# Kernel optimization log

Measured on AMD Instinct MI355X. Metric: run time of the kernel, lower is better.

The kernel has to match this reference:

```python
import jax, jax.numpy as jnp
import numpy as np

D_MODEL = 1024
N_HEADS = 16
HEAD_DIM = D_MODEL // N_HEADS
D_FF = 4 * D_MODEL
EPS = 1e-5


def layer_norm(x, gamma, beta):
    mu = jnp.mean(x, axis=-1, keepdims=True)
    var = jnp.var(x, axis=-1, keepdims=True)
    return (x - mu) * jax.lax.rsqrt(var + EPS) * gamma + beta


def setup_inputs() -> dict:
    key = jax.random.key(0)
    ks = jax.random.split(key, 12)
    B, T, S = 4, 2048, 2048
    s_in = 1.0 / np.sqrt(D_MODEL)
    s_ff = 1.0 / np.sqrt(D_FF)
    return {
        "x": jax.random.normal(ks[0], (B, T, D_MODEL), jnp.float32),
        "context": jax.random.normal(ks[1], (B, S, D_MODEL), jnp.float32),
        "Wq": jax.random.normal(ks[2], (D_MODEL, D_MODEL), jnp.float32) * s_in,
        "Wk": jax.random.normal(ks[3], (D_MODEL, D_MODEL), jnp.float32) * s_in,
        "Wv": jax.random.normal(ks[4], (D_MODEL, D_MODEL), jnp.float32) * s_in,
        "Wo": jax.random.normal(ks[5], (D_MODEL, D_MODEL), jnp.float32) * s_in,
        "W1": jax.random.normal(ks[6], (D_FF, D_MODEL), jnp.float32) * s_in,
        "W2": jax.random.normal(ks[7], (D_MODEL, D_FF), jnp.float32) * s_ff,
        "g1": jnp.ones((D_MODEL,), jnp.float32),
        "b1": jnp.zeros((D_MODEL,), jnp.float32),
        "gc": jnp.ones((D_MODEL,), jnp.float32),
        "bc": jnp.zeros((D_MODEL,), jnp.float32),
        "g2": jnp.ones((D_MODEL,), jnp.float32),
        "b2": jnp.zeros((D_MODEL,), jnp.float32),
    }


def reference(x, context, Wq, Wk, Wv, Wo, W1, W2, g1, b1, gc, bc, g2, b2):
    B, T, C = x.shape
    S = context.shape[1]
    residual = x
    xn = layer_norm(x, g1, b1)
    cn = layer_norm(context, gc, bc)
    # torch Linear: y = x @ W.T ; split heads -> [B, H, T, Dh]
    q = (xn @ Wq.T).reshape(B, T, N_HEADS, HEAD_DIM).transpose(0, 2, 1, 3)
    k = (cn @ Wk.T).reshape(B, S, N_HEADS, HEAD_DIM).transpose(0, 2, 1, 3)
    v = (cn @ Wv.T).reshape(B, S, N_HEADS, HEAD_DIM).transpose(0, 2, 1, 3)
    scale = HEAD_DIM ** (-0.5)
    attn = jax.nn.softmax(jnp.einsum('bhtd,bhsd->bhts', q, k) * scale, axis=-1)
    o = jnp.einsum('bhts,bhsd->bhtd', attn, v).transpose(0, 2, 1, 3).reshape(B, T, C)
    x = residual + o @ Wo.T
    residual = x
    h = layer_norm(x, g2, b2)
    h = jax.nn.gelu(h @ W1.T, approximate=False) @ W2.T
    return residual + h
```

## Files before the change

kernel.cpp:

```cpp
#include <hip/hip_runtime.h>
#include <cstdint>
#include <cstddef>

typedef __attribute__((ext_vector_type(8))) short short8;
typedef __attribute__((ext_vector_type(4))) short short4v;
typedef __attribute__((ext_vector_type(4))) float f32x4;
typedef __attribute__((ext_vector_type(2))) unsigned uint2v;

#define DEV static __device__ __forceinline__

DEV short f2bf(float f) {
    unsigned u = __builtin_bit_cast(unsigned, f);
    unsigned r = (u + 0x7fffu + ((u >> 16) & 1u)) >> 16;
    return (short)r;
}

DEV unsigned cvt_pk_bf16(float a, float b) {
    unsigned r;
    asm("v_cvt_pk_bf16_f32 %0, %1, %2" : "=v"(r) : "v"(a), "v"(b));
    return r;
}

DEV float exp2_hw(float x) {
    float r;
    asm("v_exp_f32 %0, %1" : "=v"(r) : "v"(x));
    return r;
}

DEV float rcp_hw(float x) {
    float r;
    asm("v_rcp_f32 %0, %1" : "=v"(r) : "v"(x));
    return r;
}

DEV float gelu_f(float v) {
    float t  = v * (1.0f + 0.044715f * v * v);
    float e  = exp2_hw(fminf(2.3022082f * t, 126.0f));
    return v * e * rcp_hw(e + 1.0f);
}

DEV void gld16(const void* g, void* l) {
    __builtin_amdgcn_global_load_lds((const __attribute__((address_space(1))) void*)g,
                                     (__attribute__((address_space(3))) void*)l, 16, 0, 0);
}

#define MFMA(c, a, b) asm volatile("v_mfma_f32_16x16x32_bf16 %0, %1, %2, %0" : "+v"(c) : "v"(a), "v"(b))
#define BAR() asm volatile("s_barrier" ::: "memory")

__global__ __launch_bounds__(256) void cvt_weights(
    const float* __restrict__ wq, const float* __restrict__ wk,
    const float* __restrict__ wv, const float* __restrict__ wo,
    const float* __restrict__ w1, const float* __restrict__ w2,
    short* __restrict__ dst) {
    long long gid = (long long)blockIdx.x * 256 + threadIdx.x;
    long long i4 = gid * 4;
    const float* src; long long loc;
    if (i4 < (4LL << 20)) {
        int s = (int)(i4 >> 20);
        src = (s == 0) ? wq : (s == 1) ? wk : (s == 2) ? wv : wo;
        loc = i4 & ((1LL << 20) - 1);
    } else {
        long long r = i4 - (4LL << 20);
        int s = (int)(r >> 22);
        src = s ? w2 : w1;
        loc = r & ((1LL << 22) - 1);
    }
    float4 v = *(const float4*)(src + loc);
    short4v o;
    o.x = f2bf(v.x); o.y = f2bf(v.y); o.z = f2bf(v.z); o.w = f2bf(v.w);
    *(short4v*)(dst + i4) = o;
}

__global__ __launch_bounds__(256) void ln_bf16(const float* __restrict__ x,
                                               const float* __restrict__ g,
                                               const float* __restrict__ bt,
                                               short* __restrict__ out) {
    int row = blockIdx.x;
    const float4* xr = (const float4*)(x + (size_t)row * 1024);
    float4 v = xr[threadIdx.x];
    float s  = v.x + v.y + v.z + v.w;
    float s2 = v.x*v.x + v.y*v.y + v.z*v.z + v.w*v.w;
    #pragma unroll
    for (int m = 1; m < 64; m <<= 1) { s += __shfl_xor(s, m); s2 += __shfl_xor(s2, m); }
    __shared__ float red[8];
    int wid = threadIdx.x >> 6;
    if ((threadIdx.x & 63) == 0) { red[wid] = s; red[4 + wid] = s2; }
    __syncthreads();
    s  = red[0] + red[1] + red[2] + red[3];
    s2 = red[4] + red[5] + red[6] + red[7];
    float mu  = s * (1.0f / 1024.0f);
    float var = fmaxf(s2 * (1.0f / 1024.0f) - mu * mu, 0.0f);
    float rs  = rsqrtf(var + 1e-5f);
    float4 gv = ((const float4*)g)[threadIdx.x];
    float4 bv = ((const float4*)bt)[threadIdx.x];
    short4v o;
    o.x = f2bf((v.x - mu) * rs * gv.x + bv.x);
    o.y = f2bf((v.y - mu) * rs * gv.y + bv.y);
    o.z = f2bf((v.z - mu) * rs * gv.z + bv.z);
    o.w = f2bf((v.w - mu) * rs * gv.w + bv.w);
    *(short4v*)(out + (size_t)row * 1024 + (size_t)threadIdx.x * 4) = o;
}

template<int MODE>
DEV void gemm_core(const short* __restrict__ A, const short* __restrict__ B,
                   void* __restrict__ out, const float* __restrict__ resid,
                   int N, int K, int lda, int ldb, float osc, int bm, int bn) {
    __shared__ short lds[2 * 32768];
    const int tid = threadIdx.x;
    const int row0 = bm << 8, col0 = bn << 8;
    const int wid = tid >> 6, lane = tid & 63;
    const int wm = wid >> 2, wn = wid & 3;
    const int lr = lane & 15, lg = lane >> 4;
    const int NK = K >> 6;

    auto stage = [&](int kt, int which) {
        int d = kt & 1;
        const short* src; int rb; int ld;
        if (which < 2) { src = A; rb = row0; ld = lda; } else { src = B; rb = col0; ld = ldb; }
        int rhalf = (which & 1) << 7;
        short* dst = lds + d * 32768 + which * 8192;
        #pragma unroll
        for (int l = 0; l < 2; ++l) {
            int g = l * 512 + tid;
            int r = g >> 3, c = g & 7;
            gld16(src + (size_t)(rb + rhalf + r) * ld + kt * 64 + ((c ^ (r & 7)) << 3),
                  dst + g * 8);
        }
    };

    f32x4 acc[8][4] = {};

    stage(0, 0); stage(0, 1); stage(0, 2); stage(0, 3);
    if (NK > 1) {
        stage(1, 2); stage(1, 3);
        asm volatile("s_waitcnt vmcnt(4)" ::: "memory");
    } else {
        asm volatile("s_waitcnt vmcnt(0)" ::: "memory");
    }
    BAR();

    const int rBbase = (wn & 1) << 6;
    for (int t = 0; t < NK; ++t) {
        const short* bufA = lds + (t & 1) * 32768 + wm * 8192;
        const short* bufB = lds + (t & 1) * 32768 + 16384 + (wn >> 1) * 8192;
        bool st1 = (t + 1) < NK, st2 = (t + 2) < NK;
        short8 bf2[2][4];

        {
            short8 af[4];
            #pragma unroll
            for (int i = 0; i < 4; ++i) {
                int r = i * 16 + lr;
                af[i] = *(const short8*)(bufA + r * 64 + ((lg ^ (r & 7)) << 3));
            }
            #pragma unroll
            for (int j = 0; j < 4; ++j) {
                int rB = rBbase + j * 16 + lr;
                bf2[0][j] = *(const short8*)(bufB + rB * 64 + ((lg ^ (rB & 7)) << 3));
            }
            if (st1) stage(t + 1, 0);
            BAR();
            __builtin_amdgcn_s_setprio(1);
            #pragma unroll
            for (int i = 0; i < 4; ++i)
                #pragma unroll
                for (int j = 0; j < 4; ++j)
                    MFMA(acc[i][j], af[i], bf2[0][j]);
            __builtin_amdgcn_s_setprio(0);
            BAR();
        }
        {
            short8 af[4];
            #pragma unroll
            for (int i = 0; i < 4; ++i) {
                int r = i * 16 + lr;
                af[i] = *(const short8*)(bufA + r * 64 + (((4 + lg) ^ (r & 7)) << 3));
            }
            #pragma unroll
            for (int j = 0; j < 4; ++j) {
                int rB = rBbase + j * 16 + lr;
                bf2[1][j] = *(const short8*)(bufB + rB * 64 + (((4 + lg) ^ (rB & 7)) << 3));
            }
            if (st1) stage(t + 1, 1);
            BAR();
            __builtin_amdgcn_s_setprio(1);
            #pragma unroll
            for (int i = 0; i < 4; ++i)
                #pragma unroll
                for (int j = 0; j < 4; ++j)
                    MFMA(acc[i][j], af[i], bf2[1][j]);
            __builtin_amdgcn_s_setprio(0);
            BAR();
        }
        {
            short8 af[4];
            #pragma unroll
            for (int i = 0; i < 4; ++i) {
                int r = 64 + i * 16 + lr;
                af[i] = *(const short8*)(bufA + r * 64 + ((lg ^ (r & 7)) << 3));
            }
            if (st2) stage(t + 2, 2);
            BAR();
            __builtin_amdgcn_s_setprio(1);
            #pragma unroll
            for (int i = 0; i < 4; ++i)
                #pragma unroll
                for (int j = 0; j < 4; ++j)
                    MFMA(acc[4 + i][j], af[i], bf2[0][j]);
            __builtin_amdgcn_s_setprio(0);
            BAR();
        }
        {
            short8 af[4];
            #pragma unroll
            for (int i = 0; i < 4; ++i) {
                int r = 64 + i * 16 + lr;
                af[i] = *(const short8*)(bufA + r * 64 + (((4 + lg) ^ (r & 7)) << 3));
            }
            if (st2) stage(t + 2, 3);
            BAR();
            __builtin_amdgcn_s_setprio(1);
            #pragma unroll
            for (int i = 0; i < 4; ++i)
                #pragma unroll
                for (int j = 0; j < 4; ++j)
                    MFMA(acc[4 + i][j], af[i], bf2[1][j]);
            __builtin_amdgcn_s_setprio(0);
            if (st2)      asm volatile("s_waitcnt vmcnt(4)" ::: "memory");
            else if (st1) asm volatile("s_waitcnt vmcnt(0)" ::: "memory");
            BAR();
        }
    }
    asm volatile("s_nop 7\n\ts_nop 7");

    int orow0 = row0 + wm * 128, ocol0 = col0 + wn * 64;
    #pragma unroll
    for (int i = 0; i < 8; ++i)
        #pragma unroll
        for (int j = 0; j < 4; ++j)
            #pragma unroll
            for (int r = 0; r < 4; ++r) {
                int gr = orow0 + i * 16 + lg * 4 + r;
                int gc = ocol0 + j * 16 + lr;
                size_t off = (size_t)gr * N + gc;
                float v = acc[i][j][r];
                if constexpr (MODE == 1) {
                    ((float*)out)[off] = resid ? v + resid[off] : v;
                } else if constexpr (MODE == 2) {
                    ((short*)out)[off] = f2bf(gelu_f(v));
                } else {
                    ((short*)out)[off] = f2bf(v * osc);
                }
            }
}

__global__ __launch_bounds__(512, 2) void gemm_qkv(
    const short* __restrict__ XN, const short* __restrict__ CN,
    const short* __restrict__ Wq, const short* __restrict__ Wk, const short* __restrict__ Wv,
    short* __restrict__ QB, short* __restrict__ KB, short* __restrict__ VT, float qscale) {
    int sid = (blockIdx.x & 7) * 48 + (blockIdx.x >> 3);
    int sub = sid >> 7, i = sid & 127;
    const short *A, *B; short* o; float osc; int N, bm, bn;
    if (sub == 0)      { A = XN; B = Wq; o = QB; osc = qscale; N = 1024; bm = i >> 2; bn = i & 3; }
    else if (sub == 1) { A = CN; B = Wk; o = KB; osc = 1.0f;   N = 1024; bm = i >> 2; bn = i & 3; }
    else               { A = Wv; B = CN; o = VT; osc = 1.0f;   N = 8192; bm = i >> 5; bn = i & 31; }
    gemm_core<3>(A, B, o, nullptr, N, 1024, 1024, 1024, osc, bm, bn);
}

template<int MODE>
__global__ __launch_bounds__(512, 2) void gemm_std(const short* __restrict__ A,
                                                   const short* __restrict__ B,
                                                   void* __restrict__ out,
                                                   const float* __restrict__ resid,
                                                   int N, int K, float osc) {
    int cpx = gridDim.x >> 3;
    int sid = (blockIdx.x & 7) * cpx + (blockIdx.x >> 3);
    int nbn = N >> 8;
    int bm = sid / nbn, bn = sid % nbn;
    gemm_core<MODE>(A, B, out, resid, N, K, K, K, osc, bm, bn);
}

__global__ __launch_bounds__(512, 2) void gemm_ff2(const short* __restrict__ F1,
                                                   const short* __restrict__ W2,
                                                   float* __restrict__ dOut,
                                                   float* __restrict__ P2,
                                                   const float* __restrict__ X2) {
    int sid = (blockIdx.x & 7) * 32 + (blockIdx.x >> 3);
    int h = sid >> 7, i = sid & 127;
    int bm = i >> 2, bn = i & 3;
    const short* A = F1 + h * 2048;
    const short* B = W2 + h * 2048;
    float* o = h ? P2 : dOut;
    const float* r = h ? nullptr : X2;
    gemm_core<1>(A, B, o, r, 1024, 2048, 4096, 4096, 1.0f, bm, bn);
}

__global__ __launch_bounds__(256) void add_f32(float* __restrict__ dst,
                                               const float* __restrict__ src, int n4) {
    int i = blockIdx.x * 256 + threadIdx.x;
    int stride = gridDim.x * 256;
    for (; i < n4; i += stride) {
        float4 a = ((const float4*)dst)[i];
        float4 b = ((const float4*)src)[i];
        a.x += b.x; a.y += b.y; a.z += b.z; a.w += b.w;
        ((float4*)dst)[i] = a;
    }
}

__global__ __launch_bounds__(512) void attn(const short* __restrict__ Q,
                                            const short* __restrict__ K,
                                            const short* __restrict__ Vt,
                                            short* __restrict__ O) {
    __shared__ short lK[2][64 * 64];
    __shared__ short lV[2][64 * 64];
    __shared__ short lP[8][32 * 64];
    int tid = threadIdx.x;
    int sid = (blockIdx.x & 7) * 64 + (blockIdx.x >> 3);
    int bh = sid >> 3, qt = sid & 7;
    int b = bh >> 4, h = bh & 15;
    int wid = tid >> 6, lane = tid & 63;
    int lr = lane & 15, lg = lane >> 4;
    int q0 = qt * 256 + wid * 32;

    short8 qf[2][2];
    #pragma unroll
    for (int fm = 0; fm < 2; ++fm)
        #pragma unroll
        for (int kb = 0; kb < 2; ++kb) {
            size_t roff = (size_t)(b * 2048 + q0 + fm * 16 + lr) * 1024 + h * 64 + kb * 32 + lg * 8;
            qf[fm][kb] = *(const short8*)(Q + roff);
        }

    f32x4 oacc[2][4] = {};
    float mrow[2] = { -1e30f, -1e30f };
    float lrs[2]  = { 0.0f, 0.0f };

    const short* Kb = K + (size_t)(b * 2048) * 1024 + h * 64;
    const short* Vb = Vt + (size_t)(h * 64) * 8192 + b * 2048;
    short* Pw = lP[wid];
    int albase = (lane & 48) >> 2;

    int sr = tid >> 3, sc = tid & 7;
    int ssl = sc ^ (sr & 7);
    auto stage = [&](int st, int d) {
        gld16(Kb + (size_t)(st * 64 + sr) * 1024 + ssl * 8, &lK[d][tid * 8]);
        gld16(Vb + (size_t)sr * 8192 + st * 64 + ssl * 8, &lV[d][tid * 8]);
    };

    stage(0, 0);
    asm volatile("s_waitcnt vmcnt(0)" ::: "memory");
    BAR();

    for (int st = 0; st < 32; ++st) {
        int d = st & 1;
        if (st + 1 < 32) stage(st + 1, d ^ 1);

        f32x4 sc2[4][2] = {};
        #pragma unroll
        for (int kb = 0; kb < 2; ++kb) {
            short8 kf[4];
            #pragma unroll
            for (int fn = 0; fn < 4; ++fn) {
                int kr = fn * 16 + lr;
                kf[fn] = *(const short8*)(lK[d] + kr * 64 + (((kb * 4 + lg) ^ (kr & 7)) << 3));
            }
            #pragma unroll
            for (int fn = 0; fn < 4; ++fn)
                #pragma unroll
                for (int fm = 0; fm < 2; ++fm)
                    MFMA(sc2[fn][fm], kf[fn], qf[fm][kb]);
        }
        asm volatile("s_nop 7\n\ts_nop 7");

        #pragma unroll
        for (int fm = 0; fm < 2; ++fm) {
            float pm = sc2[0][fm][0];
            #pragma unroll
            for (int fn = 0; fn < 4; ++fn)
                #pragma unroll
                for (int r = 0; r < 4; ++r)
                    if (fn | r) pm = fmaxf(pm, sc2[fn][fm][r]);
            pm = fmaxf(pm, __shfl_xor(pm, 16));
            pm = fmaxf(pm, __shfl_xor(pm, 32));

            float mo = mrow[fm];
            float mn = mo;
            float al = 1.0f;
            if (!__all(pm <= mo + 8.0f)) {
                mn = fmaxf(mo, pm);
                al = exp2_hw(mo - mn);
                mrow[fm] = mn;
                #pragma unroll
                for (int r = 0; r < 4; ++r) {
                    float alr = __shfl(al, albase + r);
                    #pragma unroll
                    for (int fn = 0; fn < 4; ++fn) oacc[fm][fn][r] *= alr;
                }
            }

            float p[4][4];
            float ps = 0.0f;
            #pragma unroll
            for (int fn = 0; fn < 4; ++fn)
                #pragma unroll
                for (int r = 0; r < 4; ++r) {
                    p[fn][r] = exp2_hw(sc2[fn][fm][r] - mn);
                    ps += p[fn][r];
                }
            ps += __shfl_xor(ps, 16);
            ps += __shfl_xor(ps, 32);
            lrs[fm] = lrs[fm] * al + ps;

            int pr = fm * 16 + lr;
            int swz = (pr & 7) << 3;
            #pragma unroll
            for (int fn = 0; fn < 4; ++fn) {
                uint2v w;
                w.x = cvt_pk_bf16(p[fn][0], p[fn][1]);
                w.y = cvt_pk_bf16(p[fn][2], p[fn][3]);
                *(uint2v*)(Pw + ((pr * 64 + fn * 16 + lg * 4) ^ swz)) = w;
            }
        }

        #pragma unroll
        for (int kb = 0; kb < 2; ++kb) {
            short8 pa[2], vf[4];
            #pragma unroll
            for (int fm = 0; fm < 2; ++fm) {
                int pr = fm * 16 + lr;
                pa[fm] = *(const short8*)(Pw + pr * 64 + (((kb * 4 + lg) ^ (pr & 7)) << 3));
            }
            #pragma unroll
            for (int fn = 0; fn < 4; ++fn) {
                int vr = fn * 16 + lr;
                vf[fn] = *(const short8*)(lV[d] + vr * 64 + (((kb * 4 + lg) ^ (vr & 7)) << 3));
            }
            #pragma unroll
            for (int fm = 0; fm < 2; ++fm)
                #pragma unroll
                for (int fn = 0; fn < 4; ++fn)
                    MFMA(oacc[fm][fn], pa[fm], vf[fn]);
        }

        asm volatile("s_waitcnt vmcnt(0)" ::: "memory");
        BAR();
    }
    asm volatile("s_nop 7\n\ts_nop 7");

    #pragma unroll
    for (int fm = 0; fm < 2; ++fm)
        #pragma unroll
        for (int r = 0; r < 4; ++r) {
            float linv = __shfl(lrs[fm], albase + r);
            float inv = 1.0f / linv;
            #pragma unroll
            for (int fn = 0; fn < 4; ++fn) {
                size_t off = (size_t)(b * 2048 + q0 + fm * 16 + lg * 4 + r) * 1024 + h * 64 + fn * 16 + lr;
                O[off] = f2bf(oacc[fm][fn][r] * inv);
            }
        }
}

extern "C" void kernel_launch(void* const* d_in, const int* in_sizes, int n_in,
                              void* d_out, int out_size, void* d_ws, size_t ws_size,
                              hipStream_t stream) {
    const float* x   = (const float*)d_in[0];
    const float* ctx = (const float*)d_in[1];
    const float* Wq  = (const float*)d_in[2];
    const float* Wk  = (const float*)d_in[3];
    const float* Wv  = (const float*)d_in[4];
    const float* Wo  = (const float*)d_in[5];
    const float* W1  = (const float*)d_in[6];
    const float* W2  = (const float*)d_in[7];
    const float* g1  = (const float*)d_in[8];
    const float* b1  = (const float*)d_in[9];
    const float* gc  = (const float*)d_in[10];
    const float* bc  = (const float*)d_in[11];
    const float* g2  = (const float*)d_in[12];
    const float* b2  = (const float*)d_in[13];

    char* ws = (char*)d_ws;
    const size_t OFF_W  = 0;
    const size_t OFF_XN = 25165824;
    const size_t OFF_CN = OFF_XN + 16777216;
    const size_t OFF_QB = OFF_CN + 16777216;
    const size_t OFF_KB = OFF_QB + 16777216;
    const size_t OFF_VT = OFF_KB + 16777216;
    const size_t OFF_X2 = OFF_VT + 16777216;
    const size_t OFF_F1 = OFF_X2 + 33554432;

    short* Wb = (short*)(ws + OFF_W);
    short* XN = (short*)(ws + OFF_XN);
    short* CN = (short*)(ws + OFF_CN);
    short* QB = (short*)(ws + OFF_QB);
    short* KB = (short*)(ws + OFF_KB);
    short* VT = (short*)(ws + OFF_VT);
    float* X2 = (float*)(ws + OFF_X2);
    short* F1 = (short*)(ws + OFF_F1);
    short* OB = XN;
    short* H  = CN;
    float* P2 = (float*)(ws + OFF_QB);

    const size_t WQo = 0, WKo = 1048576, WVo = 2097152, WOo = 3145728;
    const size_t W1o = 4194304, W2o = 8388608;
    const float QSCALE = 0.125f * 1.4426950408889634f;

    cvt_weights<<<12288, 256, 0, stream>>>(Wq, Wk, Wv, Wo, W1, W2, Wb);
    ln_bf16<<<8192, 256, 0, stream>>>(x, g1, b1, XN);
    ln_bf16<<<8192, 256, 0, stream>>>(ctx, gc, bc, CN);
    gemm_qkv<<<384, 512, 0, stream>>>(XN, CN, Wb + WQo, Wb + WKo, Wb + WVo, QB, KB, VT, QSCALE);
    attn<<<512, 512, 0, stream>>>(QB, KB, VT, OB);
    gemm_std<1><<<128, 512, 0, stream>>>(OB, Wb + WOo, X2, x, 1024, 1024, 1.0f);
    ln_bf16<<<8192, 256, 0, stream>>>(X2, g2, b2, H);
    gemm_std<2><<<512, 512, 0, stream>>>(H, Wb + W1o, F1, nullptr, 4096, 1024, 1.0f);
    gemm_ff2<<<256, 512, 0, stream>>>(F1, Wb + W2o, (float*)d_out, P2, X2);
    add_f32<<<2048, 256, 0, stream>>>((float*)d_out, P2, 2097152);
}
```

Measured before the change: 469.1 us.

## Halve attention query tile per wave and pass P through register shuffles

The attention kernel now gives each wave 16 query rows instead of 32 and launches twice as many blocks. The softmax probabilities are rearranged into the MFMA A-operand layout with cross-lane shuffles, so the per-wave P tile in LDS and its write/read round trip are gone. Launch bounds request higher occupancy. In exchange, each K/V tile staged in LDS feeds half as many query rows, so K/V global traffic and staging barriers per unit of work double.

```diff
diff --git a/kernel.cpp b/kernel.cpp
--- a/kernel.cpp
+++ b/kernel.cpp
@@ -5,7 +5,7 @@
 typedef __attribute__((ext_vector_type(8))) short short8;
 typedef __attribute__((ext_vector_type(4))) short short4v;
 typedef __attribute__((ext_vector_type(4))) float f32x4;
-typedef __attribute__((ext_vector_type(2))) unsigned uint2v;
+typedef __attribute__((ext_vector_type(4))) unsigned uint4v;
 
 #define DEV static __device__ __forceinline__
 
@@ -307,41 +307,38 @@
     }
 }
 
-__global__ __launch_bounds__(512) void attn(const short* __restrict__ Q,
-                                            const short* __restrict__ K,
-                                            const short* __restrict__ Vt,
-                                            short* __restrict__ O) {
+__global__ __launch_bounds__(512, 6) void attn(const short* __restrict__ Q,
+                                               const short* __restrict__ K,
+                                               const short* __restrict__ Vt,
+                                               short* __restrict__ O) {
     __shared__ short lK[2][64 * 64];
     __shared__ short lV[2][64 * 64];
-    __shared__ short lP[8][32 * 64];
     int tid = threadIdx.x;
-    int sid = (blockIdx.x & 7) * 64 + (blockIdx.x >> 3);
-    int bh = sid >> 3, qt = sid & 7;
+    int sid = (blockIdx.x & 7) * 128 + (blockIdx.x >> 3);
+    int bh = sid >> 4, qt = sid & 15;
     int b = bh >> 4, h = bh & 15;
     int wid = tid >> 6, lane = tid & 63;
     int lr = lane & 15, lg = lane >> 4;
-    int q0 = qt * 256 + wid * 32;
-
-    short8 qf[2][2];
+    int q0 = qt * 128 + wid * 16;
+    bool cbit = (lane & 16) != 0;
+    bool hihalf = (lane & 32) != 0;
+
+    short8 qf[2];
     #pragma unroll
-    for (int fm = 0; fm < 2; ++fm)
-        #pragma unroll
-        for (int kb = 0; kb < 2; ++kb) {
-            size_t roff = (size_t)(b * 2048 + q0 + fm * 16 + lr) * 1024 + h * 64 + kb * 32 + lg * 8;
-            qf[fm][kb] = *(const short8*)(Q + roff);
-        }
-
-    f32x4 oacc[2][4] = {};
-    float mrow[2] = { -1e30f, -1e30f };
-    float lrs[2]  = { 0.0f, 0.0f };
+    for (int kb = 0; kb < 2; ++kb) {
+        size_t roff = (size_t)(b * 2048 + q0 + lr) * 1024 + h * 64 + kb * 32 + lg * 8;
+        qf[kb] = *(const short8*)(Q + roff);
+    }
+
+    f32x4 oacc[4] = {};
+    float mrow = -1e30f, lsum = 0.0f;
 
     const short* Kb = K + (size_t)(b * 2048) * 1024 + h * 64;
     const short* Vb = Vt + (size_t)(h * 64) * 8192 + b * 2048;
-    short* Pw = lP[wid];
     int albase = (lane & 48) >> 2;
 
-    int sr = tid >> 3, sc = tid & 7;
-    int ssl = sc ^ (sr & 7);
+    int sr = tid >> 3, scc = tid & 7;
+    int ssl = scc ^ (sr & 7);
     auto stage = [&](int st, int d) {
         gld16(Kb + (size_t)(st * 64 + sr) * 1024 + ssl * 8, &lK[d][tid * 8]);
         gld16(Vb + (size_t)sr * 8192 + st * 64 + ssl * 8, &lV[d][tid * 8]);
@@ -355,7 +352,7 @@
         int d = st & 1;
         if (st + 1 < 32) stage(st + 1, d ^ 1);
 
-        f32x4 sc2[4][2] = {};
+        f32x4 sc2[4] = {};
         #pragma unroll
         for (int kb = 0; kb < 2; ++kb) {
             short8 kf[4];
@@ -366,80 +363,89 @@
             }
             #pragma unroll
             for (int fn = 0; fn < 4; ++fn)
+                MFMA(sc2[fn], kf[fn], qf[kb]);
+        }
+        asm volatile("s_nop 7\n\ts_nop 7");
+
+        float pm = sc2[0][0];
+        #pragma unroll
+        for (int fn = 0; fn < 4; ++fn)
+            #pragma unroll
+            for (int r = 0; r < 4; ++r)
+                if (fn | r) pm = fmaxf(pm, sc2[fn][r]);
+        pm = fmaxf(pm, __shfl_xor(pm, 16));
+        pm = fmaxf(pm, __shfl_xor(pm, 32));
+
+        float al = 1.0f;
+        float mn = mrow;
+        if (!__all(pm <= mrow + 8.0f)) {
+            mn = fmaxf(mrow, pm);
+            al = exp2_hw(mrow - mn);
+            mrow = mn;
+            #pragma unroll
+            for (int r = 0; r < 4; ++r) {
+                float alr = __shfl(al, albase + r);
                 #pragma unroll
-                for (int fm = 0; fm < 2; ++fm)
-                    MFMA(sc2[fn][fm], kf[fn], qf[fm][kb]);
-        }
-        asm volatile("s_nop 7\n\ts_nop 7");
-
-        #pragma unroll
-        for (int fm = 0; fm < 2; ++fm) {
-            float pm = sc2[0][fm][0];
-            #pragma unroll
-            for (int fn = 0; fn < 4; ++fn)
-                #pragma unroll
-                for (int r = 0; r < 4; ++r)
-                    if (fn | r) pm = fmaxf(pm, sc2[fn][fm][r]);
-            pm = fmaxf(pm, __shfl_xor(pm, 16));
-            pm = fmaxf(pm, __shfl_xor(pm, 32));
-
-            float mo = mrow[fm];
-            float mn = mo;
-            float al = 1.0f;
-            if (!__all(pm <= mo + 8.0f)) {
-                mn = fmaxf(mo, pm);
-                al = exp2_hw(mo - mn);
-                mrow[fm] = mn;
-                #pragma unroll
-                for (int r = 0; r < 4; ++r) {
-                    float alr = __shfl(al, albase + r);
-                    #pragma unroll
-                    for (int fn = 0; fn < 4; ++fn) oacc[fm][fn][r] *= alr;
-                }
-            }
-
-            float p[4][4];
-            float ps = 0.0f;
-            #pragma unroll
-            for (int fn = 0; fn < 4; ++fn)
-                #pragma unroll
-                for (int r = 0; r < 4; ++r) {
-                    p[fn][r] = exp2_hw(sc2[fn][fm][r] - mn);
-                    ps += p[fn][r];
-                }
-            ps += __shfl_xor(ps, 16);
-            ps += __shfl_xor(ps, 32);
-            lrs[fm] = lrs[fm] * al + ps;
-
-            int pr = fm * 16 + lr;
-            int swz = (pr & 7) << 3;
-            #pragma unroll
-            for (int fn = 0; fn < 4; ++fn) {
-                uint2v w;
-                w.x = cvt_pk_bf16(p[fn][0], p[fn][1]);
-                w.y = cvt_pk_bf16(p[fn][2], p[fn][3]);
-                *(uint2v*)(Pw + ((pr * 64 + fn * 16 + lg * 4) ^ swz)) = w;
-            }
+                for (int fn = 0; fn < 4; ++fn) oacc[fn][r] *= alr;
+            }
+        }
+
+        float p[4][4];
+        float ps = 0.0f;
+        #pragma unroll
+        for (int fn = 0; fn < 4; ++fn)
+            #pragma unroll
+            for (int r = 0; r < 4; ++r) {
+                p[fn][r] = exp2_hw(sc2[fn][r] - mn);
+                ps += p[fn][r];
+            }
+        ps += __shfl_xor(ps, 16);
+        ps += __shfl_xor(ps, 32);
+        lsum = lsum * al + ps;
+
+        unsigned U[4][2];
+        #pragma unroll
+        for (int fn = 0; fn < 4; ++fn) {
+            U[fn][0] = cvt_pk_bf16(p[fn][0], p[fn][1]);
+            U[fn][1] = cvt_pk_bf16(p[fn][2], p[fn][3]);
         }
 
         #pragma unroll
         for (int kb = 0; kb < 2; ++kb) {
-            short8 pa[2], vf[4];
-            #pragma unroll
-            for (int fm = 0; fm < 2; ++fm) {
-                int pr = fm * 16 + lr;
-                pa[fm] = *(const short8*)(Pw + pr * 64 + (((kb * 4 + lg) ^ (pr & 7)) << 3));
-            }
+            unsigned lo0 = U[kb * 2][0],     lo1 = U[kb * 2][1];
+            unsigned hi0 = U[kb * 2 + 1][0], hi1 = U[kb * 2 + 1][1];
+            unsigned t0 = (unsigned)__shfl_xor((int)lo0, 32);
+            unsigned t1 = (unsigned)__shfl_xor((int)lo1, 32);
+            unsigned s0 = (unsigned)__shfl_xor((int)hi0, 32);
+            unsigned s1 = (unsigned)__shfl_xor((int)hi1, 32);
+            unsigned nlo0 = hihalf ? s0 : lo0;
+            unsigned nlo1 = hihalf ? s1 : lo1;
+            unsigned nhi0 = hihalf ? hi0 : t0;
+            unsigned nhi1 = hihalf ? hi1 : t1;
+            unsigned a0 = cbit ? nhi0 : nlo0;
+            unsigned a1 = cbit ? nhi1 : nlo1;
+            unsigned x0 = (unsigned)__shfl_xor((int)nlo0, 16);
+            unsigned x1 = (unsigned)__shfl_xor((int)nlo1, 16);
+            unsigned y0 = (unsigned)__shfl_xor((int)nhi0, 16);
+            unsigned y1 = (unsigned)__shfl_xor((int)nhi1, 16);
+            unsigned b0 = cbit ? y0 : x0;
+            unsigned b1 = cbit ? y1 : x1;
+            uint4v pw;
+            pw.x = cbit ? b0 : a0;
+            pw.y = cbit ? b1 : a1;
+            pw.z = cbit ? a0 : b0;
+            pw.w = cbit ? a1 : b1;
+            short8 pa = __builtin_bit_cast(short8, pw);
+
+            short8 vf[4];
             #pragma unroll
             for (int fn = 0; fn < 4; ++fn) {
                 int vr = fn * 16 + lr;
                 vf[fn] = *(const short8*)(lV[d] + vr * 64 + (((kb * 4 + lg) ^ (vr & 7)) << 3));
             }
             #pragma unroll
-            for (int fm = 0; fm < 2; ++fm)
-                #pragma unroll
-                for (int fn = 0; fn < 4; ++fn)
-                    MFMA(oacc[fm][fn], pa[fm], vf[fn]);
+            for (int fn = 0; fn < 4; ++fn)
+                MFMA(oacc[fn], pa, vf[fn]);
         }
 
         asm volatile("s_waitcnt vmcnt(0)" ::: "memory");
@@ -448,17 +454,15 @@
     asm volatile("s_nop 7\n\ts_nop 7");
 
     #pragma unroll
-    for (int fm = 0; fm < 2; ++fm)
-        #pragma unroll
-        for (int r = 0; r < 4; ++r) {
-            float linv = __shfl(lrs[fm], albase + r);
-            float inv = 1.0f / linv;
-            #pragma unroll
-            for (int fn = 0; fn < 4; ++fn) {
-                size_t off = (size_t)(b * 2048 + q0 + fm * 16 + lg * 4 + r) * 1024 + h * 64 + fn * 16 + lr;
-                O[off] = f2bf(oacc[fm][fn][r] * inv);
-            }
-        }
+    for (int r = 0; r < 4; ++r) {
+        float linv = __shfl(lsum, albase + r);
+        float inv = 1.0f / linv;
+        #pragma unroll
+        for (int fn = 0; fn < 4; ++fn) {
+            size_t off = (size_t)(b * 2048 + q0 + lg * 4 + r) * 1024 + h * 64 + fn * 16 + lr;
+            O[off] = f2bf(oacc[fn][r] * inv);
+        }
+    }
 }
 
 extern "C" void kernel_launch(void* const* d_in, const int* in_sizes, int n_in,
@@ -509,7 +513,7 @@
     ln_bf16<<<8192, 256, 0, stream>>>(x, g1, b1, XN);
     ln_bf16<<<8192, 256, 0, stream>>>(ctx, gc, bc, CN);
     gemm_qkv<<<384, 512, 0, stream>>>(XN, CN, Wb + WQo, Wb + WKo, Wb + WVo, QB, KB, VT, QSCALE);
-    attn<<<512, 512, 0, stream>>>(QB, KB, VT, OB);
+    attn<<<1024, 512, 0, stream>>>(QB, KB, VT, OB);
     gemm_std<1><<<128, 512, 0, stream>>>(OB, Wb + WOo, X2, x, 1024, 1024, 1.0f);
     ln_bf16<<<8192, 256, 0, stream>>>(X2, g2, b2, H);
     gemm_std<2><<<512, 512, 0, stream>>>(H, Wb + W1o, F1, nullptr, 4096, 1024, 1.0f);
```

Result: no change. 467.4 us (-0.4%).

## Keep attention P in registers, fuse prep kernels, use permlane reductions

Applied to the files above, without the earlier changes.

The attention kernel no longer writes the softmax probabilities to per-wave LDS and reads them back. It packs them into MFMA A-operand registers directly and reloads V with a matching split 4-element permuted layout. Row max and sum reductions now use tree ordering and v_permlane32_swap in place of a second shuffle, and launch bounds request 4 waves per SIMD. The weight conversion and both input layernorms are merged into a single prep launch to cut launch overhead. In exchange, V reads become two half-width LDS loads per fragment, and correctness depends on the register layout matching the MFMA operand layout.

```diff
diff --git a/kernel.cpp b/kernel.cpp
--- a/kernel.cpp
+++ b/kernel.cpp
@@ -5,7 +5,7 @@
 typedef __attribute__((ext_vector_type(8))) short short8;
 typedef __attribute__((ext_vector_type(4))) short short4v;
 typedef __attribute__((ext_vector_type(4))) float f32x4;
-typedef __attribute__((ext_vector_type(2))) unsigned uint2v;
+typedef __attribute__((ext_vector_type(4))) unsigned uint4v;
 
 #define DEV static __device__ __forceinline__
 
@@ -47,35 +47,19 @@
 #define MFMA(c, a, b) asm volatile("v_mfma_f32_16x16x32_bf16 %0, %1, %2, %0" : "+v"(c) : "v"(a), "v"(b))
 #define BAR() asm volatile("s_barrier" ::: "memory")
 
-__global__ __launch_bounds__(256) void cvt_weights(
-    const float* __restrict__ wq, const float* __restrict__ wk,
-    const float* __restrict__ wv, const float* __restrict__ wo,
-    const float* __restrict__ w1, const float* __restrict__ w2,
-    short* __restrict__ dst) {
-    long long gid = (long long)blockIdx.x * 256 + threadIdx.x;
-    long long i4 = gid * 4;
-    const float* src; long long loc;
-    if (i4 < (4LL << 20)) {
-        int s = (int)(i4 >> 20);
-        src = (s == 0) ? wq : (s == 1) ? wk : (s == 2) ? wv : wo;
-        loc = i4 & ((1LL << 20) - 1);
-    } else {
-        long long r = i4 - (4LL << 20);
-        int s = (int)(r >> 22);
-        src = s ? w2 : w1;
-        loc = r & ((1LL << 22) - 1);
-    }
-    float4 v = *(const float4*)(src + loc);
-    short4v o;
-    o.x = f2bf(v.x); o.y = f2bf(v.y); o.z = f2bf(v.z); o.w = f2bf(v.w);
-    *(short4v*)(dst + i4) = o;
-}
-
-__global__ __launch_bounds__(256) void ln_bf16(const float* __restrict__ x,
-                                               const float* __restrict__ g,
-                                               const float* __restrict__ bt,
-                                               short* __restrict__ out) {
-    int row = blockIdx.x;
+DEV float red32_max(float v) {
+    float a = v, b = v;
+    asm volatile("v_permlane32_swap_b32 %0, %1" : "+v"(a), "+v"(b));
+    return fmaxf(a, b);
+}
+DEV float red32_add(float v) {
+    float a = v, b = v;
+    asm volatile("v_permlane32_swap_b32 %0, %1" : "+v"(a), "+v"(b));
+    return a + b;
+}
+
+DEV void ln_row(const float* __restrict__ x, const float* __restrict__ g,
+                const float* __restrict__ bt, short* __restrict__ out, int row) {
     const float4* xr = (const float4*)(x + (size_t)row * 1024);
     float4 v = xr[threadIdx.x];
     float s  = v.x + v.y + v.z + v.w;
@@ -101,6 +85,48 @@
     *(short4v*)(out + (size_t)row * 1024 + (size_t)threadIdx.x * 4) = o;
 }
 
+__global__ __launch_bounds__(256) void prep(
+    const float* __restrict__ wq, const float* __restrict__ wk,
+    const float* __restrict__ wv, const float* __restrict__ wo,
+    const float* __restrict__ w1, const float* __restrict__ w2,
+    short* __restrict__ dstW,
+    const float* __restrict__ x,   const float* __restrict__ g1, const float* __restrict__ b1,
+    short* __restrict__ XN,
+    const float* __restrict__ ctx, const float* __restrict__ gc, const float* __restrict__ bc,
+    short* __restrict__ CN) {
+    int bid = blockIdx.x;
+    if (bid < 12288) {
+        long long gid = (long long)bid * 256 + threadIdx.x;
+        long long i4 = gid * 4;
+        const float* src; long long loc;
+        if (i4 < (4LL << 20)) {
+            int s = (int)(i4 >> 20);
+            src = (s == 0) ? wq : (s == 1) ? wk : (s == 2) ? wv : wo;
+            loc = i4 & ((1LL << 20) - 1);
+        } else {
+            long long r = i4 - (4LL << 20);
+            int s = (int)(r >> 22);
+            src = s ? w2 : w1;
+            loc = r & ((1LL << 22) - 1);
+        }
+        float4 v = *(const float4*)(src + loc);
+        short4v o;
+        o.x = f2bf(v.x); o.y = f2bf(v.y); o.z = f2bf(v.z); o.w = f2bf(v.w);
+        *(short4v*)(dstW + i4) = o;
+    } else if (bid < 12288 + 8192) {
+        ln_row(x, g1, b1, XN, bid - 12288);
+    } else {
+        ln_row(ctx, gc, bc, CN, bid - 20480);
+    }
+}
+
+__global__ __launch_bounds__(256) void ln_bf16(const float* __restrict__ x,
+                                               const float* __restrict__ g,
+                                               const float* __restrict__ bt,
+                                               short* __restrict__ out) {
+    ln_row(x, g, bt, out, blockIdx.x);
+}
+
 template<int MODE>
 DEV void gemm_core(const short* __restrict__ A, const short* __restrict__ B,
                    void* __restrict__ out, const float* __restrict__ resid,
@@ -307,13 +333,12 @@
     }
 }
 
-__global__ __launch_bounds__(512) void attn(const short* __restrict__ Q,
-                                            const short* __restrict__ K,
-                                            const short* __restrict__ Vt,
-                                            short* __restrict__ O) {
+__global__ __launch_bounds__(512, 4) void attn(const short* __restrict__ Q,
+                                               const short* __restrict__ K,
+                                               const short* __restrict__ Vt,
+                                               short* __restrict__ O) {
     __shared__ short lK[2][64 * 64];
     __shared__ short lV[2][64 * 64];
-    __shared__ short lP[8][32 * 64];
     int tid = threadIdx.x;
     int sid = (blockIdx.x & 7) * 64 + (blockIdx.x >> 3);
     int bh = sid >> 3, qt = sid & 7;
@@ -333,15 +358,14 @@
 
     f32x4 oacc[2][4] = {};
     float mrow[2] = { -1e30f, -1e30f };
-    float lrs[2]  = { 0.0f, 0.0f };
+    float lsum[2] = { 0.0f, 0.0f };
 
     const short* Kb = K + (size_t)(b * 2048) * 1024 + h * 64;
     const short* Vb = Vt + (size_t)(h * 64) * 8192 + b * 2048;
-    short* Pw = lP[wid];
     int albase = (lane & 48) >> 2;
 
-    int sr = tid >> 3, sc = tid & 7;
-    int ssl = sc ^ (sr & 7);
+    int sr = tid >> 3, scc = tid & 7;
+    int ssl = scc ^ (sr & 7);
     auto stage = [&](int st, int d) {
         gld16(Kb + (size_t)(st * 64 + sr) * 1024 + ssl * 8, &lK[d][tid * 8]);
         gld16(Vb + (size_t)sr * 8192 + st * 64 + ssl * 8, &lV[d][tid * 8]);
@@ -372,23 +396,24 @@
         }
         asm volatile("s_nop 7\n\ts_nop 7");
 
+        short8 pa[2][2];
         #pragma unroll
         for (int fm = 0; fm < 2; ++fm) {
-            float pm = sc2[0][fm][0];
-            #pragma unroll
-            for (int fn = 0; fn < 4; ++fn)
-                #pragma unroll
-                for (int r = 0; r < 4; ++r)
-                    if (fn | r) pm = fmaxf(pm, sc2[fn][fm][r]);
+            float m8[8];
+            #pragma unroll
+            for (int i = 0; i < 8; ++i)
+                m8[i] = fmaxf(sc2[i >> 2][fm][i & 3], sc2[(i + 8) >> 2][fm][(i + 8) & 3]);
+            float ma = fmaxf(fmaxf(m8[0], m8[1]), fmaxf(m8[2], m8[3]));
+            float mb = fmaxf(fmaxf(m8[4], m8[5]), fmaxf(m8[6], m8[7]));
+            float pm = fmaxf(ma, mb);
             pm = fmaxf(pm, __shfl_xor(pm, 16));
-            pm = fmaxf(pm, __shfl_xor(pm, 32));
-
-            float mo = mrow[fm];
-            float mn = mo;
+            pm = red32_max(pm);
+
             float al = 1.0f;
-            if (!__all(pm <= mo + 8.0f)) {
-                mn = fmaxf(mo, pm);
-                al = exp2_hw(mo - mn);
+            float mn = mrow[fm];
+            if (!__all(pm <= mn + 8.0f)) {
+                mn = fmaxf(mn, pm);
+                al = exp2_hw(mrow[fm] - mn);
                 mrow[fm] = mn;
                 #pragma unroll
                 for (int r = 0; r < 4; ++r) {
@@ -399,47 +424,51 @@
             }
 
             float p[4][4];
-            float ps = 0.0f;
             #pragma unroll
             for (int fn = 0; fn < 4; ++fn)
                 #pragma unroll
-                for (int r = 0; r < 4; ++r) {
+                for (int r = 0; r < 4; ++r)
                     p[fn][r] = exp2_hw(sc2[fn][fm][r] - mn);
-                    ps += p[fn][r];
-                }
+            float s8[8];
+            #pragma unroll
+            for (int i = 0; i < 8; ++i)
+                s8[i] = p[i >> 2][i & 3] + p[(i + 8) >> 2][(i + 8) & 3];
+            float ps = ((s8[0] + s8[1]) + (s8[2] + s8[3])) + ((s8[4] + s8[5]) + (s8[6] + s8[7]));
             ps += __shfl_xor(ps, 16);
-            ps += __shfl_xor(ps, 32);
-            lrs[fm] = lrs[fm] * al + ps;
-
-            int pr = fm * 16 + lr;
-            int swz = (pr & 7) << 3;
-            #pragma unroll
-            for (int fn = 0; fn < 4; ++fn) {
-                uint2v w;
-                w.x = cvt_pk_bf16(p[fn][0], p[fn][1]);
-                w.y = cvt_pk_bf16(p[fn][2], p[fn][3]);
-                *(uint2v*)(Pw + ((pr * 64 + fn * 16 + lg * 4) ^ swz)) = w;
-            }
+            ps = red32_add(ps);
+            lsum[fm] = lsum[fm] * al + ps;
+
+            uint4v pw0, pw1;
+            pw0.x = cvt_pk_bf16(p[0][0], p[0][1]);
+            pw0.y = cvt_pk_bf16(p[0][2], p[0][3]);
+            pw0.z = cvt_pk_bf16(p[1][0], p[1][1]);
+            pw0.w = cvt_pk_bf16(p[1][2], p[1][3]);
+            pw1.x = cvt_pk_bf16(p[2][0], p[2][1]);
+            pw1.y = cvt_pk_bf16(p[2][2], p[2][3]);
+            pw1.z = cvt_pk_bf16(p[3][0], p[3][1]);
+            pw1.w = cvt_pk_bf16(p[3][2], p[3][3]);
+            pa[fm][0] = __builtin_bit_cast(short8, pw0);
+            pa[fm][1] = __builtin_bit_cast(short8, pw1);
         }
 
         #pragma unroll
         for (int kb = 0; kb < 2; ++kb) {
-            short8 pa[2], vf[4];
-            #pragma unroll
-            for (int fm = 0; fm < 2; ++fm) {
-                int pr = fm * 16 + lr;
-                pa[fm] = *(const short8*)(Pw + pr * 64 + (((kb * 4 + lg) ^ (pr & 7)) << 3));
-            }
+            short8 vf[4];
             #pragma unroll
             for (int fn = 0; fn < 4; ++fn) {
                 int vr = fn * 16 + lr;
-                vf[fn] = *(const short8*)(lV[d] + vr * 64 + (((kb * 4 + lg) ^ (vr & 7)) << 3));
-            }
-            #pragma unroll
-            for (int fm = 0; fm < 2; ++fm)
-                #pragma unroll
-                for (int fn = 0; fn < 4; ++fn)
-                    MFMA(oacc[fm][fn], pa[fm], vf[fn]);
+                int so_lo = (((kb * 4 + (lg >> 1)) ^ (vr & 7)) << 3) + ((lg & 1) << 2);
+                int so_hi = (((kb * 4 + 2 + (lg >> 1)) ^ (vr & 7)) << 3) + ((lg & 1) << 2);
+                union { short4v hv[2]; short8 v; } u;
+                u.hv[0] = *(const short4v*)(lV[d] + vr * 64 + so_lo);
+                u.hv[1] = *(const short4v*)(lV[d] + vr * 64 + so_hi);
+                vf[fn] = u.v;
+            }
+            #pragma unroll
+            for (int fn = 0; fn < 4; ++fn)
+                #pragma unroll
+                for (int fm = 0; fm < 2; ++fm)
+                    MFMA(oacc[fm][fn], pa[fm][kb], vf[fn]);
         }
 
         asm volatile("s_waitcnt vmcnt(0)" ::: "memory");
@@ -451,7 +480,7 @@
     for (int fm = 0; fm < 2; ++fm)
         #pragma unroll
         for (int r = 0; r < 4; ++r) {
-            float linv = __shfl(lrs[fm], albase + r);
+            float linv = __shfl(lsum[fm], albase + r);
             float inv = 1.0f / linv;
             #pragma unroll
             for (int fn = 0; fn < 4; ++fn) {
@@ -505,9 +534,8 @@
     const size_t W1o = 4194304, W2o = 8388608;
     const float QSCALE = 0.125f * 1.4426950408889634f;
 
-    cvt_weights<<<12288, 256, 0, stream>>>(Wq, Wk, Wv, Wo, W1, W2, Wb);
-    ln_bf16<<<8192, 256, 0, stream>>>(x, g1, b1, XN);
-    ln_bf16<<<8192, 256, 0, stream>>>(ctx, gc, bc, CN);
+    prep<<<28672, 256, 0, stream>>>(Wq, Wk, Wv, Wo, W1, W2, Wb,
+                                    x, g1, b1, XN, ctx, gc, bc, CN);
     gemm_qkv<<<384, 512, 0, stream>>>(XN, CN, Wb + WQo, Wb + WKo, Wb + WVo, QB, KB, VT, QSCALE);
     attn<<<512, 512, 0, stream>>>(QB, KB, VT, OB);
     gemm_std<1><<<128, 512, 0, stream>>>(OB, Wb + WOo, X2, x, 1024, 1024, 1.0f);
```

After: 438.6 us. 6.5% less time.
